# Performance work log

Hardware: AMD Instinct MI355X
Metric: run time of the kernel (lower is better)

Reference implementation:

```python
import jax, jax.numpy as jnp
import numpy as np


def setup_inputs() -> dict:
    key = jax.random.key(0)
    ks = jax.random.split(key, 8)
    B, C, T, V = 64, 256, 64, 25
    h = 8
    x_cls = jax.random.normal(ks[0], (B, C, 1, V), dtype=jnp.float32)
    x_patch = jax.random.normal(ks[1], (B, C, T, V), dtype=jnp.float32)
    s = 0.02
    q_w = jax.random.normal(ks[2], (C, C), dtype=jnp.float32) * s
    k_w = jax.random.normal(ks[3], (C, C), dtype=jnp.float32) * s
    v_w = jax.random.normal(ks[4], (C, C), dtype=jnp.float32) * s
    temp = jnp.ones((h, 1), dtype=jnp.float32)
    proj_w = jax.random.normal(ks[5], (C, C), dtype=jnp.float32) * s
    proj_b = jnp.zeros((C,), dtype=jnp.float32)
    return {"x_cls": x_cls, "x_patch": x_patch, "q_w": q_w, "k_w": k_w,
            "v_w": v_w, "temp": temp, "proj_w": proj_w, "proj_b": proj_b}


def reference(x_cls, x_patch, q_w, k_w, v_w, temp, proj_w, proj_b):
    B, C, _, V = x_cls.shape
    T = x_patch.shape[2]
    h = temp.shape[0]
    hd = C // h
    # (B, C, 1, V) -> (B, V, C) token layout; patches -> (B, T*V, C)
    xc = jnp.transpose(x_cls.reshape(B, C, V), (0, 2, 1))
    xp = jnp.transpose(x_patch.reshape(B, C, T * V), (0, 2, 1))
    # nn.Linear: y = x @ W.T (no bias since qkv_bias=False)
    q = (xc @ q_w.T).reshape(B, V, h, hd).transpose(0, 2, 1, 3)        # (B,h,V,hd)
    k = (xp @ k_w.T).reshape(B, T * V, h, hd).transpose(0, 2, 1, 3)    # (B,h,TV,hd)
    v = (xp @ v_w.T).reshape(B, T * V, h, hd).transpose(0, 2, 1, 3)    # (B,h,TV,hd)
    # scores: (B,h,V,TV), scaled by 1/sqrt(hd) then per-head temperature
    scale = 1.0 / jnp.sqrt(jnp.asarray(hd, dtype=q.dtype))
    attn = jnp.einsum('bhqd,bhkd->bhqk', q, k) * scale
    attn = attn * temp[None, :, :, None]  # temp (h,1) -> broadcast (1,h,1,1)
    attn = jax.nn.softmax(attn, axis=-1)
    out = jnp.einsum('bhqk,bhkd->bhqd', attn, v)                       # (B,h,V,hd)
    out = out.transpose(0, 2, 1, 3).reshape(B, V, C)
    out = out @ proj_w.T + proj_b
    return jnp.transpose(out, (0, 2, 1)).reshape(B, C, 1, V)
```

## Files before the change

kernel.cpp:

```cpp
#include <hip/hip_runtime.h>

#define B_ 64
#define C_ 256
#define TV_ 1600
#define V_ 25
#define H_ 8

typedef __attribute__((ext_vector_type(2))) int   intx2;
typedef __attribute__((ext_vector_type(4))) int   intx4;
typedef __attribute__((ext_vector_type(4))) float floatx4;
typedef __attribute__((ext_vector_type(8))) short short8;

__device__ __forceinline__ unsigned short f2bf(float f) {
    union { float f; unsigned u; } c; c.f = f;
    unsigned u = c.u;
    u += 0x7fffu + ((u >> 16) & 1u);
    return (unsigned short)(u >> 16);
}
__device__ __forceinline__ float bf2f(unsigned short s) {
    union { unsigned u; float f; } c; c.u = ((unsigned)s) << 16;
    return c.f;
}
__device__ __forceinline__ int pk_bf2(float a, float b) {
    return (int)((unsigned)f2bf(a) | ((unsigned)f2bf(b) << 16));
}

__global__ __launch_bounds__(256) void k_pre(
        const float* __restrict__ xp, unsigned short* __restrict__ XF,
        const float* __restrict__ xcls, const float* __restrict__ qw,
        const float* __restrict__ kw, const float* __restrict__ temp,
        unsigned short* __restrict__ QT,
        const float* __restrict__ vw, const float* __restrict__ pw,
        unsigned short* __restrict__ VWB, unsigned short* __restrict__ PWB) {
    __shared__ float smem[9152];
    const int blk = blockIdx.x;
    const int t = threadIdx.x;

    if (blk >= 576) {
        const int blkk = blk - 576;
        const int b = blkk / 25, nb = blkk - b * 25;
        const int n0 = nb * 64;
        const int n = t & 63, cq = t >> 6;
        const float* xb = xp + (size_t)b * C_ * TV_ + n0 + n;
        const size_t cb0 = (size_t)(b * 50 + nb * 2 + (n >> 5)) * 1024 + (n & 31);
        #pragma unroll 2
        for (int j4 = 0; j4 < 8; j4++) {
            const int cg = cq * 8 + j4;
            const float* src = xb + (size_t)(cg * 8) * TV_;
            float f[8];
            #pragma unroll
            for (int k = 0; k < 8; k++) f[k] = src[(size_t)k * TV_];
            intx4 w;
            w[0] = pk_bf2(f[0], f[1]);
            w[1] = pk_bf2(f[2], f[3]);
            w[2] = pk_bf2(f[4], f[5]);
            w[3] = pk_bf2(f[6], f[7]);
            *(intx4*)(XF + (cb0 + (size_t)cg * 32) * 8) = w;
        }
    } else if (blk < 512) {
        float* xq  = smem;
        float* kws = smem;
        float* qh  = smem + 8320;
        const int b = blk >> 3, h = blk & 7;
        {
            const float* src = xcls + ((size_t)(b * C_ + t)) * V_;
            #pragma unroll
            for (int q = 0; q < V_; q++) xq[q * 260 + t] = src[q];
        }
        __syncthreads();
        floatx4 kreg[8];
        {
            const float* krow = kw + (size_t)(h * 32 + (t >> 3)) * C_ + (t & 7) * 32;
            #pragma unroll
            for (int j = 0; j < 8; j++) kreg[j] = *(const floatx4*)(krow + 4 * j);
        }
        for (int idx = t; idx < 800; idx += 256) {
            const int q = idx >> 5, d = idx & 31;
            const float* qwr = qw + (size_t)(h * 32 + d) * C_;
            float acc = 0.f;
            #pragma unroll 4
            for (int c4 = 0; c4 < 64; c4++) {
                const floatx4 a = *(const floatx4*)(qwr + 4 * c4);
                const floatx4 x = *(const floatx4*)&xq[q * 260 + 4 * c4];
                acc += a[0] * x[0] + a[1] * x[1] + a[2] * x[2] + a[3] * x[3];
            }
            qh[q * 33 + d] = acc;
        }
        __syncthreads();
        {
            float* kdst = kws + (t >> 3) * 260 + (t & 7) * 32;
            #pragma unroll
            for (int j = 0; j < 8; j++) *(floatx4*)(kdst + 4 * j) = kreg[j];
        }
        __syncthreads();
        const float scale = temp[h] * 0.17677669529663689f * 1.4426950408889634f;
        const int qp = t & 31, cg = t >> 5;
        const int c0 = cg * 32;
        if (qp < 25) {
            floatx4 a4[8];
            #pragma unroll
            for (int j = 0; j < 8; j++) a4[j] = (floatx4){0.f, 0.f, 0.f, 0.f};
            for (int d = 0; d < 32; d++) {
                const float a = qh[qp * 33 + d];
                #pragma unroll
                for (int j4 = 0; j4 < 8; j4++) {
                    const floatx4 k4 = *(const floatx4*)&kws[d * 260 + c0 + 4 * j4];
                    a4[j4][0] += a * k4[0]; a4[j4][1] += a * k4[1];
                    a4[j4][2] += a * k4[2]; a4[j4][3] += a * k4[3];
                }
            }
            unsigned short* dst = QT + ((size_t)((b * H_ + h) * 25 + qp)) * C_ + c0;
            #pragma unroll
            for (int j8 = 0; j8 < 4; j8++) {
                intx4 w;
                w[0] = pk_bf2(scale * a4[j8 * 2][0],     scale * a4[j8 * 2][1]);
                w[1] = pk_bf2(scale * a4[j8 * 2][2],     scale * a4[j8 * 2][3]);
                w[2] = pk_bf2(scale * a4[j8 * 2 + 1][0], scale * a4[j8 * 2 + 1][1]);
                w[3] = pk_bf2(scale * a4[j8 * 2 + 1][2], scale * a4[j8 * 2 + 1][3]);
                *(intx4*)(dst + j8 * 8) = w;
            }
        }
    } else {
        const int g = (blk - 512) * 256 + t;
        const floatx4 v = ((const floatx4*)vw)[g];
        const floatx4 p = ((const floatx4*)pw)[g];
        ((intx2*)VWB)[g] = (intx2){pk_bf2(v[0], v[1]), pk_bf2(v[2], v[3])};
        ((intx2*)PWB)[g] = (intx2){pk_bf2(p[0], p[1]), pk_bf2(p[2], p[3])};
    }
}

__global__ __launch_bounds__(512, 2) void k2_attn(
        const unsigned short* __restrict__ XF, const unsigned short* __restrict__ QT,
        const unsigned short* __restrict__ VWB, float* __restrict__ OAP,
        float* __restrict__ LP) {
    __shared__ unsigned short Xs[2][8192];
    __shared__ unsigned short Ps[8][32 * 40];
    __shared__ unsigned short Vs[8][32 * 40];

    const int blk = blockIdx.x;
    const int b = blk & 63, s = blk >> 6;
    const int tid = threadIdx.x;
    const int h = tid >> 6;
    const int lane = tid & 63;
    const int quad = lane >> 4, l16 = lane & 15;

    short8 qf[2][8];
    {
        const unsigned short* qb = QT + (size_t)(b * H_ + h) * 25 * C_;
        #pragma unroll
        for (int mt = 0; mt < 2; mt++)
            #pragma unroll
            for (int ks = 0; ks < 8; ks++)
                qf[mt][ks] = *(const short8*)(qb + (mt * 16 + l16) * C_ + ks * 32 + quad * 8);
    }
    short8 vwf[2][8];
    #pragma unroll
    for (int dt = 0; dt < 2; dt++)
        #pragma unroll
        for (int ks = 0; ks < 8; ks++)
            vwf[dt][ks] = *(const short8*)(VWB + (size_t)(h * 32 + dt * 16 + l16) * C_ + ks * 32 + quad * 8);

    floatx4 oc[2][2];
    #pragma unroll
    for (int mt = 0; mt < 2; mt++)
        #pragma unroll
        for (int dt = 0; dt < 2; dt++) oc[mt][dt] = (floatx4){0.f, 0.f, 0.f, 0.f};
    float lsum[2][4];
    #pragma unroll
    for (int mt = 0; mt < 2; mt++)
        #pragma unroll
        for (int r = 0; r < 4; r++) lsum[mt][r] = 0.f;

    const unsigned short* xf_base = XF + (size_t)(b * 50 + s * 5) * 1024 * 8;
    intx4 px0 = *(const intx4*)(xf_base + (size_t)(tid * 2 + 0) * 8);
    intx4 px1 = *(const intx4*)(xf_base + (size_t)(tid * 2 + 1) * 8);
    *(intx4*)&Xs[0][(tid * 2 + 0) * 8] = px0;
    *(intx4*)&Xs[0][(tid * 2 + 1) * 8] = px1;
    __syncthreads();

    for (int ti = 0; ti < 5; ti++) {
        const int cur = ti & 1;
        if (ti < 4) {
            const unsigned short* nxt = xf_base + (size_t)(ti + 1) * 1024 * 8;
            px0 = *(const intx4*)(nxt + (size_t)(tid * 2 + 0) * 8);
            px1 = *(const intx4*)(nxt + (size_t)(tid * 2 + 1) * 8);
        }
        const unsigned short* xsc = Xs[cur];
        floatx4 sc[2][2], va[2][2];
        #pragma unroll
        for (int i = 0; i < 2; i++)
            #pragma unroll
            for (int j = 0; j < 2; j++) {
                sc[i][j] = (floatx4){0.f, 0.f, 0.f, 0.f};
                va[i][j] = (floatx4){0.f, 0.f, 0.f, 0.f};
            }
        #pragma unroll
        for (int ks = 0; ks < 8; ks++) {
            const short8 xf0 = *(const short8*)&xsc[(((ks * 4 + quad) * 32) + l16) * 8];
            const short8 xf1 = *(const short8*)&xsc[(((ks * 4 + quad) * 32) + 16 + l16) * 8];
            sc[0][0] = __builtin_amdgcn_mfma_f32_16x16x32_bf16(qf[0][ks], xf0, sc[0][0], 0, 0, 0);
            sc[0][1] = __builtin_amdgcn_mfma_f32_16x16x32_bf16(qf[0][ks], xf1, sc[0][1], 0, 0, 0);
            sc[1][0] = __builtin_amdgcn_mfma_f32_16x16x32_bf16(qf[1][ks], xf0, sc[1][0], 0, 0, 0);
            sc[1][1] = __builtin_amdgcn_mfma_f32_16x16x32_bf16(qf[1][ks], xf1, sc[1][1], 0, 0, 0);
            va[0][0] = __builtin_amdgcn_mfma_f32_16x16x32_bf16(xf0, vwf[0][ks], va[0][0], 0, 0, 0);
            va[0][1] = __builtin_amdgcn_mfma_f32_16x16x32_bf16(xf0, vwf[1][ks], va[0][1], 0, 0, 0);
            va[1][0] = __builtin_amdgcn_mfma_f32_16x16x32_bf16(xf1, vwf[0][ks], va[1][0], 0, 0, 0);
            va[1][1] = __builtin_amdgcn_mfma_f32_16x16x32_bf16(xf1, vwf[1][ks], va[1][1], 0, 0, 0);
        }
        #pragma unroll
        for (int mt = 0; mt < 2; mt++)
            #pragma unroll
            for (int g = 0; g < 2; g++)
                #pragma unroll
                for (int r = 0; r < 4; r++) {
                    const float p = __builtin_amdgcn_exp2f(sc[mt][g][r]);
                    lsum[mt][r] += p;
                    Ps[h][(mt * 16 + quad * 4 + r) * 40 + g * 16 + l16] = f2bf(p);
                }
        #pragma unroll
        for (int g = 0; g < 2; g++)
            #pragma unroll
            for (int dt = 0; dt < 2; dt++)
                *(intx2*)&Vs[h][(dt * 16 + l16) * 40 + g * 16 + quad * 4] =
                    (intx2){pk_bf2(va[g][dt][0], va[g][dt][1]),
                            pk_bf2(va[g][dt][2], va[g][dt][3])};
        #pragma unroll
        for (int mt = 0; mt < 2; mt++) {
            const short8 pa = *(const short8*)&Ps[h][(mt * 16 + l16) * 40 + quad * 8];
            #pragma unroll
            for (int dt = 0; dt < 2; dt++) {
                const short8 vb = *(const short8*)&Vs[h][(dt * 16 + l16) * 40 + quad * 8];
                oc[mt][dt] = __builtin_amdgcn_mfma_f32_16x16x32_bf16(pa, vb, oc[mt][dt], 0, 0, 0);
            }
        }
        if (ti < 4) {
            *(intx4*)&Xs[cur ^ 1][(tid * 2 + 0) * 8] = px0;
            *(intx4*)&Xs[cur ^ 1][(tid * 2 + 1) * 8] = px1;
        }
        __syncthreads();
    }
    #pragma unroll
    for (int mt = 0; mt < 2; mt++)
        #pragma unroll
        for (int r = 0; r < 4; r++) {
            float v = lsum[mt][r];
            #pragma unroll
            for (int off = 1; off < 16; off <<= 1) v += __shfl_xor(v, off, 64);
            lsum[mt][r] = v;
        }
    const size_t bh = (size_t)(b * H_ + h);
    if (l16 == 0) {
        #pragma unroll
        for (int mt = 0; mt < 2; mt++)
            #pragma unroll
            for (int r = 0; r < 4; r++) {
                const int q = mt * 16 + quad * 4 + r;
                LP[bh * 320 + s * 32 + q] = lsum[mt][r];
            }
    }
    #pragma unroll
    for (int mt = 0; mt < 2; mt++)
        #pragma unroll
        for (int dt = 0; dt < 2; dt++)
            #pragma unroll
            for (int r = 0; r < 4; r++) {
                const int q = mt * 16 + quad * 4 + r;
                if (q < 25)
                    OAP[((size_t)(bh * 25 + q)) * 320 + s * 32 + dt * 16 + l16] = oc[mt][dt][r];
            }
}

__global__ __launch_bounds__(256) void k3_proj(const float* __restrict__ OAP,
        const float* __restrict__ LP, const unsigned short* __restrict__ PWB,
        const float* __restrict__ pb, float* __restrict__ y) {
    __shared__ unsigned short OB[32 * 264];
    __shared__ float rl_s[256];
    const int blk = blockIdx.x;
    const int b = blk & 63, i0 = (blk >> 6) * 64;
    const int t = threadIdx.x;
    const int wv = t >> 6, lane = t & 63;
    const int quad = lane >> 4, l16 = lane & 15;
    {
        const int h = t >> 5, q = t & 31;
        const float* lp = LP + (size_t)(b * H_ + h) * 320 + q;
        float lv = 0.f;
        #pragma unroll
        for (int s = 0; s < 10; s++) lv += lp[s * 32];
        rl_s[t] = (q < 25) ? 1.0f / lv : 0.0f;
    }
    __syncthreads();
    for (int idx = t; idx < 8192; idx += 256) {
        const int q = idx >> 8, j = idx & 255;
        const int h2 = j >> 5, d = j & 31;
        float val = 0.f;
        if (q < 25) {
            const float* op = OAP + ((size_t)(b * H_ + h2) * 25 + q) * 320 + d;
            float acc = 0.f;
            #pragma unroll
            for (int s = 0; s < 10; s++) acc += op[s * 32];
            val = acc * rl_s[h2 * 32 + q];
        }
        OB[q * 264 + j] = f2bf(val);
    }
    __syncthreads();
    floatx4 oc[2];
    oc[0] = (floatx4){0.f, 0.f, 0.f, 0.f};
    oc[1] = (floatx4){0.f, 0.f, 0.f, 0.f};
    const int i = i0 + wv * 16 + l16;
    #pragma unroll
    for (int ks = 0; ks < 8; ks++) {
        const short8 a0 = *(const short8*)&OB[l16 * 264 + ks * 32 + quad * 8];
        const short8 a1 = *(const short8*)&OB[(16 + l16) * 264 + ks * 32 + quad * 8];
        const short8 bv = *(const short8*)(PWB + (size_t)i * C_ + ks * 32 + quad * 8);
        oc[0] = __builtin_amdgcn_mfma_f32_16x16x32_bf16(a0, bv, oc[0], 0, 0, 0);
        oc[1] = __builtin_amdgcn_mfma_f32_16x16x32_bf16(a1, bv, oc[1], 0, 0, 0);
    }
    const float bias = pb[i];
    #pragma unroll
    for (int mt = 0; mt < 2; mt++)
        #pragma unroll
        for (int r = 0; r < 4; r++) {
            const int q = mt * 16 + quad * 4 + r;
            if (q < 25) y[(size_t)b * 6400 + i * 25 + q] = oc[mt][r] + bias;
        }
}

extern "C" void kernel_launch(void* const* d_in, const int* in_sizes, int n_in,
                              void* d_out, int out_size, void* d_ws, size_t ws_size,
                              hipStream_t stream) {
    const float* xcls = (const float*)d_in[0];
    const float* xp   = (const float*)d_in[1];
    const float* qw   = (const float*)d_in[2];
    const float* kw   = (const float*)d_in[3];
    const float* vw   = (const float*)d_in[4];
    const float* temp = (const float*)d_in[5];
    const float* pw   = (const float*)d_in[6];
    const float* pb   = (const float*)d_in[7];
    float* y = (float*)d_out;

    if (ws_size < (size_t)76292096) return;
    char* ws = (char*)d_ws;
    unsigned short* XF  = (unsigned short*)ws;
    unsigned short* QT  = (unsigned short*)(ws + 52428800);
    float*          OAP = (float*)(ws + 58990592);
    float*          LP  = (float*)(ws + 75374592);
    unsigned short* VWB = (unsigned short*)(ws + 76029952);
    unsigned short* PWB = (unsigned short*)(ws + 76161024);

    hipLaunchKernelGGL(k_pre,   dim3(2176), dim3(256), 0, stream,
                       xp, XF, xcls, qw, kw, temp, QT, vw, pw, VWB, PWB);
    hipLaunchKernelGGL(k2_attn, dim3(640),  dim3(512), 0, stream, XF, QT, VWB, OAP, LP);
    hipLaunchKernelGGL(k3_proj, dim3(256),  dim3(256), 0, stream, OAP, LP, PWB, pb, y);
}
```

Baseline: 267.8 us.

## Fuse x_patch bf16 conversion into attention kernel, drop XF staging buffer

Removes the pre-pass blocks that converted x_patch to a bf16 tiled buffer (XF). The attention kernel now loads fp32 x_patch directly with float2 loads, packs to bf16 in registers, and stores it to the shared-memory double buffer. This avoids writing and re-reading the 52MB intermediate. In exchange the global loads are strided across channels with only 8-byte chunks per thread, and there is more conversion ALU work inside the attention loop.

Result: no change. 269.4 us (+0.6%).

```diff
diff --git a/kernel.cpp b/kernel.cpp
--- a/kernel.cpp
+++ b/kernel.cpp
@@ -8,6 +8,7 @@
 
 typedef __attribute__((ext_vector_type(2))) int   intx2;
 typedef __attribute__((ext_vector_type(4))) int   intx4;
+typedef __attribute__((ext_vector_type(2))) float floatx2;
 typedef __attribute__((ext_vector_type(4))) float floatx4;
 typedef __attribute__((ext_vector_type(8))) short short8;
 
@@ -17,16 +18,11 @@
     u += 0x7fffu + ((u >> 16) & 1u);
     return (unsigned short)(u >> 16);
 }
-__device__ __forceinline__ float bf2f(unsigned short s) {
-    union { unsigned u; float f; } c; c.u = ((unsigned)s) << 16;
-    return c.f;
-}
 __device__ __forceinline__ int pk_bf2(float a, float b) {
     return (int)((unsigned)f2bf(a) | ((unsigned)f2bf(b) << 16));
 }
 
 __global__ __launch_bounds__(256) void k_pre(
-        const float* __restrict__ xp, unsigned short* __restrict__ XF,
         const float* __restrict__ xcls, const float* __restrict__ qw,
         const float* __restrict__ kw, const float* __restrict__ temp,
         unsigned short* __restrict__ QT,
@@ -36,28 +32,7 @@
     const int blk = blockIdx.x;
     const int t = threadIdx.x;
 
-    if (blk >= 576) {
-        const int blkk = blk - 576;
-        const int b = blkk / 25, nb = blkk - b * 25;
-        const int n0 = nb * 64;
-        const int n = t & 63, cq = t >> 6;
-        const float* xb = xp + (size_t)b * C_ * TV_ + n0 + n;
-        const size_t cb0 = (size_t)(b * 50 + nb * 2 + (n >> 5)) * 1024 + (n & 31);
-        #pragma unroll 2
-        for (int j4 = 0; j4 < 8; j4++) {
-            const int cg = cq * 8 + j4;
-            const float* src = xb + (size_t)(cg * 8) * TV_;
-            float f[8];
-            #pragma unroll
-            for (int k = 0; k < 8; k++) f[k] = src[(size_t)k * TV_];
-            intx4 w;
-            w[0] = pk_bf2(f[0], f[1]);
-            w[1] = pk_bf2(f[2], f[3]);
-            w[2] = pk_bf2(f[4], f[5]);
-            w[3] = pk_bf2(f[6], f[7]);
-            *(intx4*)(XF + (cb0 + (size_t)cg * 32) * 8) = w;
-        }
-    } else if (blk < 512) {
+    if (blk < 512) {
         float* xq  = smem;
         float* kws = smem;
         float* qh  = smem + 8320;
@@ -130,7 +105,7 @@
 }
 
 __global__ __launch_bounds__(512, 2) void k2_attn(
-        const unsigned short* __restrict__ XF, const unsigned short* __restrict__ QT,
+        const float* __restrict__ xp, const unsigned short* __restrict__ QT,
         const unsigned short* __restrict__ VWB, float* __restrict__ OAP,
         float* __restrict__ LP) {
     __shared__ unsigned short Xs[2][8192];
@@ -144,6 +119,9 @@
     const int lane = tid & 63;
     const int quad = lane >> 4, l16 = lane & 15;
 
+    const float* xrow = xp + (size_t)b * C_ * TV_ + (size_t)((tid >> 4) * 8) * TV_
+                      + s * 160 + (tid & 15) * 2;
+
     short8 qf[2][8];
     {
         const unsigned short* qb = QT + (size_t)(b * H_ + h) * 25 * C_;
@@ -171,19 +149,26 @@
         #pragma unroll
         for (int r = 0; r < 4; r++) lsum[mt][r] = 0.f;
 
-    const unsigned short* xf_base = XF + (size_t)(b * 50 + s * 5) * 1024 * 8;
-    intx4 px0 = *(const intx4*)(xf_base + (size_t)(tid * 2 + 0) * 8);
-    intx4 px1 = *(const intx4*)(xf_base + (size_t)(tid * 2 + 1) * 8);
-    *(intx4*)&Xs[0][(tid * 2 + 0) * 8] = px0;
-    *(intx4*)&Xs[0][(tid * 2 + 1) * 8] = px1;
+    floatx2 pf[8];
+    #pragma unroll
+    for (int j = 0; j < 8; j++) pf[j] = *(const floatx2*)(xrow + (size_t)j * TV_);
+    {
+        intx4 w0, w1;
+        w0[0] = pk_bf2(pf[0][0], pf[1][0]); w0[1] = pk_bf2(pf[2][0], pf[3][0]);
+        w0[2] = pk_bf2(pf[4][0], pf[5][0]); w0[3] = pk_bf2(pf[6][0], pf[7][0]);
+        w1[0] = pk_bf2(pf[0][1], pf[1][1]); w1[1] = pk_bf2(pf[2][1], pf[3][1]);
+        w1[2] = pk_bf2(pf[4][1], pf[5][1]); w1[3] = pk_bf2(pf[6][1], pf[7][1]);
+        *(intx4*)&Xs[0][(tid * 2 + 0) * 8] = w0;
+        *(intx4*)&Xs[0][(tid * 2 + 1) * 8] = w1;
+    }
     __syncthreads();
 
     for (int ti = 0; ti < 5; ti++) {
         const int cur = ti & 1;
         if (ti < 4) {
-            const unsigned short* nxt = xf_base + (size_t)(ti + 1) * 1024 * 8;
-            px0 = *(const intx4*)(nxt + (size_t)(tid * 2 + 0) * 8);
-            px1 = *(const intx4*)(nxt + (size_t)(tid * 2 + 1) * 8);
+            #pragma unroll
+            for (int j = 0; j < 8; j++)
+                pf[j] = *(const floatx2*)(xrow + (ti + 1) * 32 + (size_t)j * TV_);
         }
         const unsigned short* xsc = Xs[cur];
         floatx4 sc[2][2], va[2][2];
@@ -234,8 +219,13 @@
             }
         }
         if (ti < 4) {
-            *(intx4*)&Xs[cur ^ 1][(tid * 2 + 0) * 8] = px0;
-            *(intx4*)&Xs[cur ^ 1][(tid * 2 + 1) * 8] = px1;
+            intx4 w0, w1;
+            w0[0] = pk_bf2(pf[0][0], pf[1][0]); w0[1] = pk_bf2(pf[2][0], pf[3][0]);
+            w0[2] = pk_bf2(pf[4][0], pf[5][0]); w0[3] = pk_bf2(pf[6][0], pf[7][0]);
+            w1[0] = pk_bf2(pf[0][1], pf[1][1]); w1[1] = pk_bf2(pf[2][1], pf[3][1]);
+            w1[2] = pk_bf2(pf[4][1], pf[5][1]); w1[3] = pk_bf2(pf[6][1], pf[7][1]);
+            *(intx4*)&Xs[cur ^ 1][(tid * 2 + 0) * 8] = w0;
+            *(intx4*)&Xs[cur ^ 1][(tid * 2 + 1) * 8] = w1;
         }
         __syncthreads();
     }
@@ -338,17 +328,16 @@
     const float* pb   = (const float*)d_in[7];
     float* y = (float*)d_out;
 
-    if (ws_size < (size_t)76292096) return;
+    if (ws_size < (size_t)23863296) return;
     char* ws = (char*)d_ws;
-    unsigned short* XF  = (unsigned short*)ws;
-    unsigned short* QT  = (unsigned short*)(ws + 52428800);
-    float*          OAP = (float*)(ws + 58990592);
-    float*          LP  = (float*)(ws + 75374592);
-    unsigned short* VWB = (unsigned short*)(ws + 76029952);
-    unsigned short* PWB = (unsigned short*)(ws + 76161024);
-
-    hipLaunchKernelGGL(k_pre,   dim3(2176), dim3(256), 0, stream,
-                       xp, XF, xcls, qw, kw, temp, QT, vw, pw, VWB, PWB);
-    hipLaunchKernelGGL(k2_attn, dim3(640),  dim3(512), 0, stream, XF, QT, VWB, OAP, LP);
-    hipLaunchKernelGGL(k3_proj, dim3(256),  dim3(256), 0, stream, OAP, LP, PWB, pb, y);
-}
+    unsigned short* QT  = (unsigned short*)ws;
+    float*          OAP = (float*)(ws + 6561792);
+    float*          LP  = (float*)(ws + 22945792);
+    unsigned short* VWB = (unsigned short*)(ws + 23601152);
+    unsigned short* PWB = (unsigned short*)(ws + 23732224);
+
+    hipLaunchKernelGGL(k_pre,   dim3(576), dim3(256), 0, stream,
+                       xcls, qw, kw, temp, QT, vw, pw, VWB, PWB);
+    hipLaunchKernelGGL(k2_attn, dim3(640), dim3(512), 0, stream, xp, QT, VWB, OAP, LP);
+    hipLaunchKernelGGL(k3_proj, dim3(256), dim3(256), 0, stream, OAP, LP, PWB, pb, y);
+}
```
